# Performance work log

Measured on AMD Instinct MI355X. Metric: run time of the kernel, lower is better.

The kernel has to match this reference:

```python
import jax, jax.numpy as jnp
import numpy as np

N_NODES = 50000
N_EDGES = 800000
IN_DIM, FEAT_DIM, HID_DIM, OUT_DIM = 512, 256, 256, 128


def _glorot(key, shape):
    fan_in = shape[-1]
    bound = 1.0 / np.sqrt(fan_in)
    return jax.random.uniform(key, shape, jnp.float32, -bound, bound)


def setup_inputs() -> dict:
    key = jax.random.key(0)
    ks = jax.random.split(key, 12)
    x = jax.random.normal(ks[0], (N_NODES, IN_DIM), jnp.float32)
    edge_index = jax.random.randint(ks[1], (2, N_EDGES), 0, N_NODES, jnp.int64)
    return {
        "x": x,
        "edge_index": edge_index,
        # feature_pre MLP
        "W_pre": _glorot(ks[2], (FEAT_DIM, IN_DIM)),
        "b_pre": jnp.zeros((FEAT_DIM,), jnp.float32),
        "W_pre2": _glorot(ks[3], (HID_DIM, FEAT_DIM)),
        "b_pre2": jnp.zeros((HID_DIM,), jnp.float32),
        # conv_first: SAGEConv(hidden, hidden); lin_l (neighbors, with bias), lin_r (root, no bias)
        "Wl1": _glorot(ks[4], (HID_DIM, HID_DIM)),
        "bl1": jnp.zeros((HID_DIM,), jnp.float32),
        "Wr1": _glorot(ks[5], (HID_DIM, HID_DIM)),
        # conv_out: SAGEConv(hidden, output)
        "Wl2": _glorot(ks[6], (OUT_DIM, HID_DIM)),
        "bl2": jnp.zeros((OUT_DIM,), jnp.float32),
        "Wr2": _glorot(ks[7], (OUT_DIM, HID_DIM)),
    }


def sage_conv(x, src, dst, Wl, bl, Wr):
    # mean-aggregate source features at destination nodes, then linear + root linear
    n = x.shape[0]
    msg = x[src]                                               # [E, D]
    agg = jax.ops.segment_sum(msg, dst, num_segments=n)        # [N, D]
    cnt = jax.ops.segment_sum(jnp.ones((src.shape[0],), x.dtype), dst, num_segments=n)
    mean = agg / jnp.maximum(cnt, 1.0)[:, None]
    return mean @ Wl.T + bl + x @ Wr.T


def reference(x, edge_index, W_pre, b_pre, W_pre2, b_pre2, Wl1, bl1, Wr1, Wl2, bl2, Wr2):
    src, dst = edge_index[0], edge_index[1]
    h = x @ W_pre.T + b_pre
    h = h @ W_pre2.T + b_pre2
    h = jax.nn.relu(sage_conv(h, src, dst, Wl1, bl1, Wr1))
    # dropout is identity in eval mode; layer_num=2 -> no hidden convs
    h = sage_conv(h, src, dst, Wl2, bl2, Wr2)
    # F.normalize(p=2, dim=-1), eps=1e-12
    norm = jnp.maximum(jnp.linalg.norm(h, axis=-1, keepdims=True), 1e-12)
    return h / norm
```

## Files before the change

### kernel.cpp

```cpp
#include <hip/hip_runtime.h>
#include <hip/hip_bf16.h>


typedef __attribute__((ext_vector_type(4))) float f32x4;
typedef __attribute__((ext_vector_type(8))) short s8v;

__device__ __forceinline__ float bf2f(unsigned short u) {
  union { unsigned int i; float f; } v; v.i = ((unsigned int)u) << 16; return v.f;
}
__device__ __forceinline__ unsigned short f2bf(float f) {
  unsigned int u = __builtin_bit_cast(unsigned int, f);
  u += 0x7fffu + ((u >> 16) & 1u);
  return (unsigned short)(u >> 16);
}

__global__ __launch_bounds__(256) void zero_int_kernel(int* __restrict__ p, int n) {
  int i = blockIdx.x * blockDim.x + threadIdx.x;
  const int stride = gridDim.x * blockDim.x;
  for (; i < n; i += stride) p[i] = 0;
}

__global__ __launch_bounds__(256) void count_kernel(const int* __restrict__ dst,
                                                    int* __restrict__ cnt, int E) {
  const int e = blockIdx.x * blockDim.x + threadIdx.x;
  if (e < E) atomicAdd(&cnt[dst[e]], 1);
}

__global__ __launch_bounds__(256) void scan_pass1(const int* __restrict__ cnt,
                                                  int* __restrict__ bsum, int M) {
  __shared__ int red[256];
  const int t = threadIdx.x;
  const int i = blockIdx.x * 256 + t;
  red[t] = (i < M) ? cnt[i] : 0;
  __syncthreads();
  for (int off = 128; off > 0; off >>= 1) {
    if (t < off) red[t] += red[t + off];
    __syncthreads();
  }
  if (t == 0) bsum[blockIdx.x] = red[0];
}

__global__ __launch_bounds__(256) void scan_pass2(const int* __restrict__ bsum,
    int* __restrict__ boff, int* __restrict__ rowptr, int nb, int M, int E) {
  __shared__ int buf[256];
  const int t = threadIdx.x;
  const int v = (t < nb) ? bsum[t] : 0;
  buf[t] = v;
  __syncthreads();
  for (int off = 1; off < 256; off <<= 1) {
    const int add = (t >= off) ? buf[t - off] : 0;
    __syncthreads();
    buf[t] += add;
    __syncthreads();
  }
  if (t < nb) boff[t] = buf[t] - v;
  if (t == 0) rowptr[M] = E;
}

__global__ __launch_bounds__(256) void scan_pass3(int* __restrict__ cnt,
    const int* __restrict__ boff, int* __restrict__ rowptr, int M) {
  __shared__ int buf[256];
  const int t = threadIdx.x;
  const int i = blockIdx.x * 256 + t;
  const int v = (i < M) ? cnt[i] : 0;
  buf[t] = v;
  __syncthreads();
  for (int off = 1; off < 256; off <<= 1) {
    const int add = (t >= off) ? buf[t - off] : 0;
    __syncthreads();
    buf[t] += add;
    __syncthreads();
  }
  if (i < M) {
    rowptr[i] = buf[t] - v + boff[blockIdx.x];
    cnt[i] = 0;
  }
}

__global__ __launch_bounds__(256) void fill_kernel(const int* __restrict__ src,
    const int* __restrict__ dst, const int* __restrict__ rowptr,
    int* __restrict__ cursor, unsigned short* __restrict__ eidx, int E) {
  const int e = blockIdx.x * blockDim.x + threadIdx.x;
  if (e >= E) return;
  const int d = dst[e];
  const int pos = rowptr[d] + atomicAdd(&cursor[d], 1);
  eidx[pos] = (unsigned short)src[e];
}

__global__ __launch_bounds__(256) void prep_kernel(const float* __restrict__ Wp,
    const float* __restrict__ Wp2, const float* __restrict__ bp,
    const float* __restrict__ bp2, const float* __restrict__ Wl1,
    const float* __restrict__ Wr1, const float* __restrict__ Wl2,
    const float* __restrict__ Wr2, unsigned short* __restrict__ Wc,
    float* __restrict__ bc, unsigned short* __restrict__ Bc1,
    unsigned short* __restrict__ Bc2) {
  const int b = blockIdx.x, t = threadIdx.x;
  if (b < 256) {
    __shared__ float wrow[256];
    wrow[t] = Wp2[b * 256 + t];
    __syncthreads();
    float a0 = 0.f, a1 = 0.f;
    for (int m = 0; m < 256; ++m) {
      const float w = wrow[m];
      a0 = fmaf(w, Wp[m * 512 + t], a0);
      a1 = fmaf(w, Wp[m * 512 + 256 + t], a1);
    }
    Wc[b * 512 + t] = f2bf(a0);
    Wc[b * 512 + 256 + t] = f2bf(a1);
  } else if (b == 256) {
    float s = 0.f;
    for (int m = 0; m < 256; ++m) s = fmaf(Wp2[t * 256 + m], bp[m], s);
    bc[t] = s + bp2[t];
  } else if (b < 769) {
    const int idx = (b - 257) * 256 + t;
    const int o = idx >> 9, k = idx & 511;
    const float v = (k < 256) ? Wl1[o * 256 + k] : Wr1[o * 256 + (k - 256)];
    Bc1[idx] = f2bf(v);
  } else {
    const int idx = (b - 769) * 256 + t;
    const int r = idx >> 8, k = idx & 255;
    const float v = (r < 128) ? Wl2[r * 256 + k] : Wr2[(r - 128) * 256 + k];
    Bc2[idx] = f2bf(v);
  }
}

#define BUF_SZ 16384

template <int K, int ASTRIDE, int CSTRIDE, int CBASE, bool BIAS_EN, bool RELU_EN, bool A_FP32>
__global__ __launch_bounds__(256) void mfma_gemm(const void* __restrict__ Ap,
    const unsigned short* __restrict__ Bp, const float* __restrict__ bias,
    unsigned short* __restrict__ Cp, int M, int nwg) {
  constexpr int NT = K / 32;
  __shared__ __align__(16) char smem[2 * BUF_SZ];

  const int xcd = blockIdx.x & 7, idx = blockIdx.x >> 3;
  const int q = nwg >> 3, r = nwg & 7;
  const int wg = (xcd < r ? xcd * (q + 1) : r * (q + 1) + (xcd - r) * q) + idx;
  const int bm = (wg >> 1) * 128;
  const int bn = (wg & 1) * 128;

  const int t = threadIdx.x, w = t >> 6, l = t & 63;
  const int wr = (w >> 1) * 64, wc = (w & 1) * 64;
  const int lane15 = l & 15, half = l >> 4;

  const int sr = t >> 2;
  const int sp = t & 3;
  const int fr = t >> 1;
  const int fh = t & 1;
  const int frow = min(bm + fr, M - 1);

  float bias_l[4];
  if (BIAS_EN) {
#pragma unroll
    for (int ns = 0; ns < 4; ++ns) bias_l[ns] = bias[bn + wc + ns * 16 + lane15];
  }

  f32x4 acc[4][4];
#pragma unroll
  for (int i = 0; i < 4; ++i)
#pragma unroll
    for (int j = 0; j < 4; ++j) acc[i][j] = f32x4{0.f, 0.f, 0.f, 0.f};

  auto stageB = [&](int buf, int k0) {
#pragma unroll
    for (int j = 0; j < 2; ++j) {
      const int rr = j * 64 + sr;
      const int sl = sp ^ ((rr >> 1) & 3);
      const unsigned short* bp = Bp + (size_t)(bn + rr) * K + k0 + sl * 8;
      __builtin_amdgcn_global_load_lds((const unsigned int*)bp,
          (unsigned int*)(smem + buf * BUF_SZ + 8192 + j * 4096 + w * 1024), 16, 0, 0);
    }
  };
  auto stageA_bf16 = [&](int buf, int k0) {
#pragma unroll
    for (int j = 0; j < 2; ++j) {
      const int rr = j * 64 + sr;
      const int sl = sp ^ ((rr >> 1) & 3);
      const unsigned short* ap = (const unsigned short*)Ap +
          (size_t)min(bm + rr, M - 1) * ASTRIDE + k0 + sl * 8;
      __builtin_amdgcn_global_load_lds((const unsigned int*)ap,
          (unsigned int*)(smem + buf * BUF_SZ + j * 4096 + w * 1024), 16, 0, 0);
    }
  };
  auto loadA_f32 = [&](int k0, float4* ar) {
    const float* ap = (const float*)Ap + (size_t)frow * ASTRIDE + k0 + fh * 16;
    ar[0] = *(const float4*)(ap + 0);
    ar[1] = *(const float4*)(ap + 4);
    ar[2] = *(const float4*)(ap + 8);
    ar[3] = *(const float4*)(ap + 12);
  };
  auto writeA_f32 = [&](int buf, const float4* ar) {
    s8v p0, p1;
    p0[0] = (short)f2bf(ar[0].x); p0[1] = (short)f2bf(ar[0].y);
    p0[2] = (short)f2bf(ar[0].z); p0[3] = (short)f2bf(ar[0].w);
    p0[4] = (short)f2bf(ar[1].x); p0[5] = (short)f2bf(ar[1].y);
    p0[6] = (short)f2bf(ar[1].z); p0[7] = (short)f2bf(ar[1].w);
    p1[0] = (short)f2bf(ar[2].x); p1[1] = (short)f2bf(ar[2].y);
    p1[2] = (short)f2bf(ar[2].z); p1[3] = (short)f2bf(ar[2].w);
    p1[4] = (short)f2bf(ar[3].x); p1[5] = (short)f2bf(ar[3].y);
    p1[6] = (short)f2bf(ar[3].z); p1[7] = (short)f2bf(ar[3].w);
    const int s0 = (2 * fh + 0) ^ ((fr >> 1) & 3);
    const int s1 = (2 * fh + 1) ^ ((fr >> 1) & 3);
    char* base = smem + buf * BUF_SZ + fr * 64;
    *(s8v*)(base + s0 * 16) = p0;
    *(s8v*)(base + s1 * 16) = p1;
  };

  if (A_FP32) {
    float4 ar[4];
    loadA_f32(0, ar);
    writeA_f32(0, ar);
  } else {
    stageA_bf16(0, 0);
  }
  stageB(0, 0);
  __syncthreads();

  int cur = 0;
#pragma unroll 2
  for (int tt = 0; tt < NT; ++tt) {
    const bool more = (tt + 1 < NT);
    float4 ar[4];
    if (more) {
      if (A_FP32) loadA_f32((tt + 1) * 32, ar);
      else stageA_bf16(cur ^ 1, (tt + 1) * 32);
      stageB(cur ^ 1, (tt + 1) * 32);
    }

    char* const Ab = smem + cur * BUF_SZ;
    char* const Bb = Ab + 8192;
    s8v af[4], bv[4];
#pragma unroll
    for (int ms = 0; ms < 4; ++ms) {
      const int rr = wr + ms * 16 + lane15;
      af[ms] = *(const s8v*)(Ab + rr * 64 + ((half ^ ((rr >> 1) & 3)) << 4));
    }
#pragma unroll
    for (int ns = 0; ns < 4; ++ns) {
      const int rr = wc + ns * 16 + lane15;
      bv[ns] = *(const s8v*)(Bb + rr * 64 + ((half ^ ((rr >> 1) & 3)) << 4));
    }
#pragma unroll
    for (int ms = 0; ms < 4; ++ms)
#pragma unroll
      for (int ns = 0; ns < 4; ++ns)
        acc[ms][ns] =
            __builtin_amdgcn_mfma_f32_16x16x32_bf16(af[ms], bv[ns], acc[ms][ns], 0, 0, 0);

    if (more) {
      if (A_FP32) writeA_f32(cur ^ 1, ar);
      __syncthreads();
    }
    cur ^= 1;
  }

#pragma unroll
  for (int ms = 0; ms < 4; ++ms)
#pragma unroll
    for (int ns = 0; ns < 4; ++ns) {
      const int col = bn + wc + ns * 16 + lane15;
      f32x4 v = acc[ms][ns];
      if (BIAS_EN) {
#pragma unroll
        for (int rg = 0; rg < 4; ++rg) v[rg] += bias_l[ns];
      }
      if (RELU_EN) {
#pragma unroll
        for (int rg = 0; rg < 4; ++rg) v[rg] = fmaxf(v[rg], 0.f);
      }
#pragma unroll
      for (int rg = 0; rg < 4; ++rg) {
        const int row = bm + wr + ms * 16 + half * 4 + rg;
        if (row < M) Cp[(size_t)row * CSTRIDE + CBASE + col] = f2bf(v[rg]);
      }
    }
}

__global__ __launch_bounds__(256) void gather_mean256_kernel(
    unsigned short* __restrict__ Acat, const int* __restrict__ rowptr,
    const unsigned short* __restrict__ eidx, int M) {
  const int node = blockIdx.x * 4 + (threadIdx.x >> 6);
  if (node >= M) return;
  const int lane = threadIdx.x & 63;
  const int c4 = lane * 4;
  const int beg = rowptr[node], end = rowptr[node + 1];
  float a0 = 0.f, a1 = 0.f, a2 = 0.f, a3 = 0.f;
  int j = beg;
  for (; j + 3 < end; j += 4) {
    const size_t s0 = eidx[j], s1 = eidx[j + 1], s2 = eidx[j + 2], s3 = eidx[j + 3];
    const ushort4 v0 = *(const ushort4*)(Acat + s0 * 512 + 256 + c4);
    const ushort4 v1 = *(const ushort4*)(Acat + s1 * 512 + 256 + c4);
    const ushort4 v2 = *(const ushort4*)(Acat + s2 * 512 + 256 + c4);
    const ushort4 v3 = *(const ushort4*)(Acat + s3 * 512 + 256 + c4);
    a0 += (bf2f(v0.x) + bf2f(v1.x)) + (bf2f(v2.x) + bf2f(v3.x));
    a1 += (bf2f(v0.y) + bf2f(v1.y)) + (bf2f(v2.y) + bf2f(v3.y));
    a2 += (bf2f(v0.z) + bf2f(v1.z)) + (bf2f(v2.z) + bf2f(v3.z));
    a3 += (bf2f(v0.w) + bf2f(v1.w)) + (bf2f(v2.w) + bf2f(v3.w));
  }
  for (; j < end; ++j) {
    const size_t s0 = eidx[j];
    const ushort4 v0 = *(const ushort4*)(Acat + s0 * 512 + 256 + c4);
    a0 += bf2f(v0.x); a1 += bf2f(v0.y); a2 += bf2f(v0.z); a3 += bf2f(v0.w);
  }
  const float inv = 1.0f / fmaxf((float)(end - beg), 1.0f);
  ushort4 o;
  o.x = f2bf(a0 * inv); o.y = f2bf(a1 * inv);
  o.z = f2bf(a2 * inv); o.w = f2bf(a3 * inv);
  *(ushort4*)(Acat + (size_t)node * 512 + c4) = o;
}

__global__ __launch_bounds__(256) void gather_finalize_kernel(
    const unsigned short* __restrict__ Acat, const int* __restrict__ rowptr,
    const unsigned short* __restrict__ eidx, const float* __restrict__ bl2,
    float* __restrict__ out, int M) {
  const int node = blockIdx.x * 4 + (threadIdx.x >> 6);
  if (node >= M) return;
  const int lane = threadIdx.x & 63;
  const int c2 = lane * 2;
  const int beg = rowptr[node], end = rowptr[node + 1];
  float ax = 0.f, ay = 0.f;
  int j = beg;
  for (; j + 3 < end; j += 4) {
    const size_t s0 = eidx[j], s1 = eidx[j + 1], s2 = eidx[j + 2], s3 = eidx[j + 3];
    const ushort2 v0 = *(const ushort2*)(Acat + s0 * 512 + 256 + c2);
    const ushort2 v1 = *(const ushort2*)(Acat + s1 * 512 + 256 + c2);
    const ushort2 v2 = *(const ushort2*)(Acat + s2 * 512 + 256 + c2);
    const ushort2 v3 = *(const ushort2*)(Acat + s3 * 512 + 256 + c2);
    ax += (bf2f(v0.x) + bf2f(v1.x)) + (bf2f(v2.x) + bf2f(v3.x));
    ay += (bf2f(v0.y) + bf2f(v1.y)) + (bf2f(v2.y) + bf2f(v3.y));
  }
  for (; j < end; ++j) {
    const size_t s0 = eidx[j];
    const ushort2 v0 = *(const ushort2*)(Acat + s0 * 512 + 256 + c2);
    ax += bf2f(v0.x); ay += bf2f(v0.y);
  }
  const float inv = 1.0f / fmaxf((float)(end - beg), 1.0f);
  const ushort2 rr = *(const ushort2*)(Acat + (size_t)node * 512 + 384 + c2);
  const float2 b = *(const float2*)&bl2[c2];
  const float vx = fmaf(ax, inv, b.x) + bf2f(rr.x);
  const float vy = fmaf(ay, inv, b.y) + bf2f(rr.y);
  float ss = vx * vx + vy * vy;
#pragma unroll
  for (int off = 32; off > 0; off >>= 1) ss += __shfl_xor(ss, off);
  const float rn = 1.0f / fmaxf(sqrtf(ss), 1e-12f);
  *(float2*)&out[(size_t)node * 128 + c2] = make_float2(vx * rn, vy * rn);
}

extern "C" void kernel_launch(void* const* d_in, const int* in_sizes, int n_in,
                              void* d_out, int out_size, void* d_ws, size_t ws_size,
                              hipStream_t stream) {
  const float* x      = (const float*)d_in[0];
  const int*   ei     = (const int*)d_in[1];
  const float* W_pre  = (const float*)d_in[2];
  const float* b_pre  = (const float*)d_in[3];
  const float* W_pre2 = (const float*)d_in[4];
  const float* b_pre2 = (const float*)d_in[5];
  const float* Wl1    = (const float*)d_in[6];
  const float* bl1    = (const float*)d_in[7];
  const float* Wr1    = (const float*)d_in[8];
  const float* Wl2    = (const float*)d_in[9];
  const float* bl2    = (const float*)d_in[10];
  const float* Wr2    = (const float*)d_in[11];
  float* out = (float*)d_out;

  const int M = in_sizes[0] / 512;
  const int E = in_sizes[1] / 2;
  const int* src = ei;
  const int* dst = ei + E;

  char* p = (char*)d_ws;
  unsigned short* Acat = (unsigned short*)p; p += (size_t)M * 512 * 2;
  unsigned short* H3   = (unsigned short*)p; p += (size_t)M * 256 * 2;
  unsigned short* Wc   = (unsigned short*)p; p += 256 * 512 * 2;
  unsigned short* Bc1  = (unsigned short*)p; p += 256 * 512 * 2;
  unsigned short* Bc2  = (unsigned short*)p; p += 256 * 256 * 2;
  float* bc   = (float*)p; p += 256 * 4;
  int* rowptr = (int*)p;   p += (size_t)(M + 1) * 4;
  int* cnt    = (int*)p;   p += (size_t)M * 4;
  int* bsum   = (int*)p;   p += 256 * 4;
  int* boff   = (int*)p;   p += 256 * 4;
  unsigned short* eidx = (unsigned short*)p;

  const int eblk = (E + 255) / 256;
  const int nb   = (M + 255) / 256;
  const int nwg  = ((M + 127) / 128) * 2;
  const int nblk = (M + 3) / 4;

  zero_int_kernel<<<256, 256, 0, stream>>>(cnt, M);
  count_kernel<<<eblk, 256, 0, stream>>>(dst, cnt, E);
  scan_pass1<<<nb, 256, 0, stream>>>(cnt, bsum, M);
  scan_pass2<<<1, 256, 0, stream>>>(bsum, boff, rowptr, nb, M, E);
  scan_pass3<<<nb, 256, 0, stream>>>(cnt, boff, rowptr, M);
  fill_kernel<<<eblk, 256, 0, stream>>>(src, dst, rowptr, cnt, eidx, E);

  prep_kernel<<<1025, 256, 0, stream>>>(W_pre, W_pre2, b_pre, b_pre2,
                                        Wl1, Wr1, Wl2, Wr2, Wc, bc, Bc1, Bc2);

  mfma_gemm<512, 512, 512, 256, true, false, true>
      <<<nwg, 256, 0, stream>>>(x, Wc, bc, Acat, M, nwg);
  gather_mean256_kernel<<<nblk, 256, 0, stream>>>(Acat, rowptr, eidx, M);
  mfma_gemm<512, 512, 256, 0, true, true, false>
      <<<nwg, 256, 0, stream>>>(Acat, Bc1, bl1, H3, M, nwg);
  mfma_gemm<256, 256, 512, 256, false, false, false>
      <<<nwg, 256, 0, stream>>>(H3, Bc2, nullptr, Acat, M, nwg);
  gather_finalize_kernel<<<nblk, 256, 0, stream>>>(Acat, rowptr, eidx, bl2, out, M);
}
```

Baseline: 286.8 us.

## Triple-buffer GEMM staging and pre-convert x to bf16 in separate kernel

Adds a standalone kernel that converts the fp32 input x to bf16 in workspace, so the first GEMM can stage A through direct global-to-LDS loads like the other GEMMs. The GEMM loop becomes a three-stage LDS ring with prefetch distance two, using explicit vmcnt waits and a single barrier per iteration instead of two buffers with a full sync. This is meant to hide more load latency and remove the register-path fp32 conversion from the GEMM. In exchange it adds an extra full pass over x (read fp32, write bf16), a larger workspace, and 48KB of LDS per block, which may lower occupancy.

New measurement: 314.8 us. +9.7%, slower.

```diff
diff --git a/kernel.cpp b/kernel.cpp
--- a/kernel.cpp
+++ b/kernel.cpp
@@ -85,6 +85,22 @@
   const int d = dst[e];
   const int pos = rowptr[d] + atomicAdd(&cursor[d], 1);
   eidx[pos] = (unsigned short)src[e];
+}
+
+__global__ __launch_bounds__(256) void cvt_x_kernel(const float* __restrict__ x,
+    unsigned short* __restrict__ xb, int n) {
+  int i = (blockIdx.x * 256 + threadIdx.x) * 8;
+  const int stride = gridDim.x * 256 * 8;
+  for (; i < n; i += stride) {
+    const float4 f0 = *(const float4*)(x + i);
+    const float4 f1 = *(const float4*)(x + i + 4);
+    s8v p;
+    p[0] = (short)f2bf(f0.x); p[1] = (short)f2bf(f0.y);
+    p[2] = (short)f2bf(f0.z); p[3] = (short)f2bf(f0.w);
+    p[4] = (short)f2bf(f1.x); p[5] = (short)f2bf(f1.y);
+    p[6] = (short)f2bf(f1.z); p[7] = (short)f2bf(f1.w);
+    *(s8v*)(xb + i) = p;
+  }
 }
 
 __global__ __launch_bounds__(256) void prep_kernel(const float* __restrict__ Wp,
@@ -124,18 +140,17 @@
   }
 }
 
-#define BUF_SZ 16384
-
-template <int K, int ASTRIDE, int CSTRIDE, int CBASE, bool BIAS_EN, bool RELU_EN, bool A_FP32>
-__global__ __launch_bounds__(256) void mfma_gemm(const void* __restrict__ Ap,
-    const unsigned short* __restrict__ Bp, const float* __restrict__ bias,
-    unsigned short* __restrict__ Cp, int M, int nwg) {
+template <int K, int ASTRIDE, int CSTRIDE, int CBASE, bool BIAS_EN, bool RELU_EN>
+__global__ __launch_bounds__(256) void mfma_gemm(
+    const unsigned short* __restrict__ Ap, const unsigned short* __restrict__ Bp,
+    const float* __restrict__ bias, unsigned short* __restrict__ Cp, int M, int nwg) {
   constexpr int NT = K / 32;
-  __shared__ __align__(16) char smem[2 * BUF_SZ];
-
-  const int xcd = blockIdx.x & 7, idx = blockIdx.x >> 3;
+  constexpr int BUF = 16384;
+  __shared__ __align__(16) char smem[3 * BUF];
+
+  const int xcd = blockIdx.x & 7, bidx = blockIdx.x >> 3;
   const int q = nwg >> 3, r = nwg & 7;
-  const int wg = (xcd < r ? xcd * (q + 1) : r * (q + 1) + (xcd - r) * q) + idx;
+  const int wg = (xcd < r ? xcd * (q + 1) : r * (q + 1) + (xcd - r) * q) + bidx;
   const int bm = (wg >> 1) * 128;
   const int bn = (wg & 1) * 128;
 
@@ -143,17 +158,15 @@
   const int wr = (w >> 1) * 64, wc = (w & 1) * 64;
   const int lane15 = l & 15, half = l >> 4;
 
-  const int sr = t >> 2;
-  const int sp = t & 3;
-  const int fr = t >> 1;
-  const int fh = t & 1;
-  const int frow = min(bm + fr, M - 1);
-
-  float bias_l[4];
-  if (BIAS_EN) {
-#pragma unroll
-    for (int ns = 0; ns < 4; ++ns) bias_l[ns] = bias[bn + wc + ns * 16 + lane15];
-  }
+  const int sr = t >> 2, sp = t & 3;
+  const int ar0 = min(bm + sr, M - 1);
+  const int ar1 = min(bm + 64 + sr, M - 1);
+  const int sl0 = sp ^ ((sr >> 1) & 3);
+  const int sl1 = sp ^ (((64 + sr) >> 1) & 3);
+  const unsigned short* apb0 = Ap + (size_t)ar0 * ASTRIDE + sl0 * 8;
+  const unsigned short* apb1 = Ap + (size_t)ar1 * ASTRIDE + sl1 * 8;
+  const unsigned short* bpb0 = Bp + (size_t)(bn + sr) * K + sl0 * 8;
+  const unsigned short* bpb1 = Bp + (size_t)(bn + 64 + sr) * K + sl1 * 8;
 
   f32x4 acc[4][4];
 #pragma unroll
@@ -161,74 +174,19 @@
 #pragma unroll
     for (int j = 0; j < 4; ++j) acc[i][j] = f32x4{0.f, 0.f, 0.f, 0.f};
 
-  auto stageB = [&](int buf, int k0) {
-#pragma unroll
-    for (int j = 0; j < 2; ++j) {
-      const int rr = j * 64 + sr;
-      const int sl = sp ^ ((rr >> 1) & 3);
-      const unsigned short* bp = Bp + (size_t)(bn + rr) * K + k0 + sl * 8;
-      __builtin_amdgcn_global_load_lds((const unsigned int*)bp,
-          (unsigned int*)(smem + buf * BUF_SZ + 8192 + j * 4096 + w * 1024), 16, 0, 0);
-    }
+  auto stage = [&](int bufOff, int k0) {
+    __builtin_amdgcn_global_load_lds((const unsigned int*)(apb0 + k0),
+        (unsigned int*)(smem + bufOff + w * 1024), 16, 0, 0);
+    __builtin_amdgcn_global_load_lds((const unsigned int*)(apb1 + k0),
+        (unsigned int*)(smem + bufOff + 4096 + w * 1024), 16, 0, 0);
+    __builtin_amdgcn_global_load_lds((const unsigned int*)(bpb0 + k0),
+        (unsigned int*)(smem + bufOff + 8192 + w * 1024), 16, 0, 0);
+    __builtin_amdgcn_global_load_lds((const unsigned int*)(bpb1 + k0),
+        (unsigned int*)(smem + bufOff + 12288 + w * 1024), 16, 0, 0);
   };
-  auto stageA_bf16 = [&](int buf, int k0) {
-#pragma unroll
-    for (int j = 0; j < 2; ++j) {
-      const int rr = j * 64 + sr;
-      const int sl = sp ^ ((rr >> 1) & 3);
-      const unsigned short* ap = (const unsigned short*)Ap +
-          (size_t)min(bm + rr, M - 1) * ASTRIDE + k0 + sl * 8;
-      __builtin_amdgcn_global_load_lds((const unsigned int*)ap,
-          (unsigned int*)(smem + buf * BUF_SZ + j * 4096 + w * 1024), 16, 0, 0);
-    }
-  };
-  auto loadA_f32 = [&](int k0, float4* ar) {
-    const float* ap = (const float*)Ap + (size_t)frow * ASTRIDE + k0 + fh * 16;
-    ar[0] = *(const float4*)(ap + 0);
-    ar[1] = *(const float4*)(ap + 4);
-    ar[2] = *(const float4*)(ap + 8);
-    ar[3] = *(const float4*)(ap + 12);
-  };
-  auto writeA_f32 = [&](int buf, const float4* ar) {
-    s8v p0, p1;
-    p0[0] = (short)f2bf(ar[0].x); p0[1] = (short)f2bf(ar[0].y);
-    p0[2] = (short)f2bf(ar[0].z); p0[3] = (short)f2bf(ar[0].w);
-    p0[4] = (short)f2bf(ar[1].x); p0[5] = (short)f2bf(ar[1].y);
-    p0[6] = (short)f2bf(ar[1].z); p0[7] = (short)f2bf(ar[1].w);
-    p1[0] = (short)f2bf(ar[2].x); p1[1] = (short)f2bf(ar[2].y);
-    p1[2] = (short)f2bf(ar[2].z); p1[3] = (short)f2bf(ar[2].w);
-    p1[4] = (short)f2bf(ar[3].x); p1[5] = (short)f2bf(ar[3].y);
-    p1[6] = (short)f2bf(ar[3].z); p1[7] = (short)f2bf(ar[3].w);
-    const int s0 = (2 * fh + 0) ^ ((fr >> 1) & 3);
-    const int s1 = (2 * fh + 1) ^ ((fr >> 1) & 3);
-    char* base = smem + buf * BUF_SZ + fr * 64;
-    *(s8v*)(base + s0 * 16) = p0;
-    *(s8v*)(base + s1 * 16) = p1;
-  };
-
-  if (A_FP32) {
-    float4 ar[4];
-    loadA_f32(0, ar);
-    writeA_f32(0, ar);
-  } else {
-    stageA_bf16(0, 0);
-  }
-  stageB(0, 0);
-  __syncthreads();
-
-  int cur = 0;
-#pragma unroll 2
-  for (int tt = 0; tt < NT; ++tt) {
-    const bool more = (tt + 1 < NT);
-    float4 ar[4];
-    if (more) {
-      if (A_FP32) loadA_f32((tt + 1) * 32, ar);
-      else stageA_bf16(cur ^ 1, (tt + 1) * 32);
-      stageB(cur ^ 1, (tt + 1) * 32);
-    }
-
-    char* const Ab = smem + cur * BUF_SZ;
-    char* const Bb = Ab + 8192;
+  auto compute = [&](int bufOff) {
+    const char* Ab = smem + bufOff;
+    const char* Bb = Ab + 8192;
     s8v af[4], bv[4];
 #pragma unroll
     for (int ms = 0; ms < 4; ++ms) {
@@ -246,14 +204,32 @@
       for (int ns = 0; ns < 4; ++ns)
         acc[ms][ns] =
             __builtin_amdgcn_mfma_f32_16x16x32_bf16(af[ms], bv[ns], acc[ms][ns], 0, 0, 0);
-
-    if (more) {
-      if (A_FP32) writeA_f32(cur ^ 1, ar);
-      __syncthreads();
-    }
-    cur ^= 1;
-  }
-
+  };
+
+  stage(0, 0);
+  stage(BUF, 32);
+
+  int offC = 0, offI = 2 * BUF;
+#pragma unroll 1
+  for (int tt = 0; tt < NT - 1; ++tt) {
+    asm volatile("s_waitcnt vmcnt(4)" ::: "memory");
+    __builtin_amdgcn_sched_barrier(0);
+    __builtin_amdgcn_s_barrier();
+    if (tt + 2 < NT) stage(offI, (tt + 2) * 32);
+    compute(offC);
+    offC = (offC == 2 * BUF) ? 0 : offC + BUF;
+    offI = (offI == 2 * BUF) ? 0 : offI + BUF;
+  }
+  asm volatile("s_waitcnt vmcnt(0)" ::: "memory");
+  __builtin_amdgcn_sched_barrier(0);
+  __builtin_amdgcn_s_barrier();
+  compute(offC);
+
+  float bias_l[4];
+  if (BIAS_EN) {
+#pragma unroll
+    for (int ns = 0; ns < 4; ++ns) bias_l[ns] = bias[bn + wc + ns * 16 + lane15];
+  }
 #pragma unroll
   for (int ms = 0; ms < 4; ++ms)
 #pragma unroll
@@ -371,6 +347,7 @@
   char* p = (char*)d_ws;
   unsigned short* Acat = (unsigned short*)p; p += (size_t)M * 512 * 2;
   unsigned short* H3   = (unsigned short*)p; p += (size_t)M * 256 * 2;
+  unsigned short* xb   = (unsigned short*)p; p += (size_t)M * 512 * 2;
   unsigned short* Wc   = (unsigned short*)p; p += 256 * 512 * 2;
   unsigned short* Bc1  = (unsigned short*)p; p += 256 * 512 * 2;
   unsigned short* Bc2  = (unsigned short*)p; p += 256 * 256 * 2;
@@ -386,6 +363,8 @@
   const int nwg  = ((M + 127) / 128) * 2;
   const int nblk = (M + 3) / 4;
 
+  cvt_x_kernel<<<2048, 256, 0, stream>>>(x, xb, M * 512);
+
   zero_int_kernel<<<256, 256, 0, stream>>>(cnt, M);
   count_kernel<<<eblk, 256, 0, stream>>>(dst, cnt, E);
   scan_pass1<<<nb, 256, 0, stream>>>(cnt, bsum, M);
@@ -396,12 +375,12 @@
   prep_kernel<<<1025, 256, 0, stream>>>(W_pre, W_pre2, b_pre, b_pre2,
                                         Wl1, Wr1, Wl2, Wr2, Wc, bc, Bc1, Bc2);
 
-  mfma_gemm<512, 512, 512, 256, true, false, true>
-      <<<nwg, 256, 0, stream>>>(x, Wc, bc, Acat, M, nwg);
+  mfma_gemm<512, 512, 512, 256, true, false>
+      <<<nwg, 256, 0, stream>>>(xb, Wc, bc, Acat, M, nwg);
   gather_mean256_kernel<<<nblk, 256, 0, stream>>>(Acat, rowptr, eidx, M);
-  mfma_gemm<512, 512, 256, 0, true, true, false>
+  mfma_gemm<512, 512, 256, 0, true, true>
       <<<nwg, 256, 0, stream>>>(Acat, Bc1, bl1, H3, M, nwg);
-  mfma_gemm<256, 256, 512, 256, false, false, false>
+  mfma_gemm<256, 256, 512, 256, false, false>
       <<<nwg, 256, 0, stream>>>(H3, Bc2, nullptr, Acat, M, nwg);
   gather_finalize_kernel<<<nblk, 256, 0, stream>>>(Acat, rowptr, eidx, bl2, out, M);
 }
```
